# Optimization experiments

Hardware: AMD Instinct MI355X
Metric: run time of the kernel (lower is better)

Reference implementation:

```python
import jax, jax.numpy as jnp
import numpy as np
import math

B, Q, D = 1, 1024, 4096
H, KV, HD = 32, 8, 128
GROUP_FACTOR, LABEL_BITS, HEAVY_CONST = 8, 4, 256
ROPE_THETA = 10000.0
NEG = jnp.finfo(jnp.float32).min


def setup_inputs() -> dict:
    key = jax.random.key(0)
    ks = jax.random.split(key, 5)
    hidden_states = jax.random.normal(ks[0], (B, Q, D), jnp.float32)
    Wq = jax.random.normal(ks[1], (D, H * HD), jnp.float32) * 0.02
    Wk = jax.random.normal(ks[2], (D, KV * HD), jnp.float32) * 0.02
    Wv = jax.random.normal(ks[3], (D, KV * HD), jnp.float32) * 0.02
    Wo = jax.random.normal(ks[4], (H * HD, D), jnp.float32) * 0.02
    # additive causal mask [B,1,Q,Q]
    causal = jnp.tril(jnp.ones((Q, Q), bool))
    attention_mask = jnp.where(causal, 0.0, NEG)[None, None].astype(jnp.float32)
    position_ids = jnp.arange(Q, dtype=jnp.int64 if jax.config.jax_enable_x64 else jnp.int32)[None]
    # per-head channel permutation (sorted channel importance order)
    rng = np.random.default_rng(0)
    sorted_channel = jnp.asarray(np.stack([rng.permutation(HD) for _ in range(H)]), jnp.int32)
    return {"hidden_states": hidden_states, "attention_mask": attention_mask,
            "position_ids": position_ids, "Wq": Wq, "Wk": Wk, "Wv": Wv, "Wo": Wo,
            "sorted_channel": sorted_channel}


def pseudo_quantize(t, q_bit):
    max_quant = 2 ** q_bit - 1
    mn = jnp.min(t, axis=-1, keepdims=True)
    mx = jnp.max(t, axis=-1, keepdims=True)
    rng = mx - mn
    rng = jnp.where(rng == 0, 1.0, rng)
    scale = max_quant / rng
    quant = jnp.clip(jnp.round((t - mn) * scale), 0, max_quant)
    return quant / scale + mn


def rotate_half(x):
    x1, x2 = jnp.split(x, 2, axis=-1)
    return jnp.concatenate([-x2, x1], axis=-1)


def _forward(hidden_states, attention_mask, Wq, Wk, Wv, Wo, position_ids, sorted_channel):
    bsz, q_len, _ = hidden_states.shape
    q = (hidden_states @ Wq).reshape(bsz, q_len, H, HD).transpose(0, 2, 1, 3)   # [B,H,Q,HD]
    k = (hidden_states @ Wk).reshape(bsz, q_len, KV, HD).transpose(0, 2, 1, 3)  # [B,KV,Q,HD]
    v = (hidden_states @ Wv).reshape(bsz, q_len, KV, HD).transpose(0, 2, 1, 3)
    kv_len = q_len

    # RoPE
    inv_freq = 1.0 / (ROPE_THETA ** (jnp.arange(0, HD, 2, dtype=jnp.float32) / HD))
    freqs = position_ids.astype(jnp.float32)[..., None] * inv_freq  # [B,Q,HD/2]
    emb = jnp.concatenate([freqs, freqs], axis=-1)
    cos = jnp.cos(emb)[:, None]  # [B,1,Q,HD]
    sin = jnp.sin(emb)[:, None]
    q = q * cos + rotate_half(q) * sin
    k = k * cos + rotate_half(k) * sin
    prev_q = q  # upper_layer_embedding is None -> previous_query_states == query_states

    # GQA repeat
    groups = H // KV
    k = jnp.repeat(k, groups, axis=1)  # [B,H,K,HD]
    v = jnp.repeat(v, groups, axis=1)

    attn = jnp.einsum('bhqd,bhkd->bhqk', q, k) / math.sqrt(HD)

    # channel gather per head (sorted_channel: [H,HD] permutation)
    idx = jnp.broadcast_to(sorted_channel[None, :, None, :], q.shape)
    sq = jnp.take_along_axis(prev_q, idx, axis=-1)
    sk = jnp.take_along_axis(k, jnp.broadcast_to(sorted_channel[None, :, None, :], k.shape), axis=-1)
    outlier = HD // GROUP_FACTOR
    gq = sq[..., :outlier]
    gk = sk[..., :outlier]
    if LABEL_BITS < 16:
        gq = pseudo_quantize(gq, LABEL_BITS)
        gk = pseudo_quantize(gk, LABEL_BITS)
    gattn = jnp.einsum('bhqd,bhkd->bhqk', gq, gk) / math.sqrt(outlier)

    attn = attn + attention_mask
    gattn = gattn + attention_mask

    # keep top heavy_const positions per query by grouped score (descending)
    rank = jnp.argsort(jnp.argsort(-gattn, axis=-1), axis=-1)
    attn = jnp.where(rank < HEAVY_CONST, attn, -jnp.inf)

    w = jax.nn.softmax(attn.astype(jnp.float32), axis=-1).astype(v.dtype)
    out = jnp.einsum('bhqk,bhkd->bhqd', w, v)
    out = out.transpose(0, 2, 1, 3).reshape(bsz, q_len, H * HD)
    return out @ Wo


def reference(hidden_states, attention_mask, position_ids, Wq, Wk, Wv, Wo, sorted_channel):
    return _forward(hidden_states, attention_mask, Wq, Wk, Wv, Wo, position_ids, sorted_channel)
```

## Files before the change

kernel.cpp:

```cpp
#include <hip/hip_runtime.h>
#include <hip/hip_bf16.h>
#include <math.h>


typedef __hip_bfloat16 bf16;
typedef unsigned short ushort_t;
typedef __attribute__((ext_vector_type(8))) short short8;
typedef __attribute__((ext_vector_type(4))) float f32x4;

#define QL   1024
#define DM   4096
#define NH   32
#define NKV  8
#define GRP  4
#define HD   128
#define OUTL 16
#define HC   256
#define MNEG (-1.0e30f)

__device__ __forceinline__ unsigned mapf(float f) {
  unsigned u = __float_as_uint(f);
  return (u & 0x80000000u) ? ~u : (u | 0x80000000u);
}

__device__ __forceinline__ unsigned short f2bf(float x) {
  unsigned u = __float_as_uint(x);
  unsigned r = (u + 0x7FFFu + ((u >> 16) & 1u)) >> 16;
  return (unsigned short)r;
}
__device__ __forceinline__ float bf2f(unsigned short h) {
  return __uint_as_float(((unsigned)h) << 16);
}

__device__ __forceinline__ short8 cvt8(const float* p) {
  f32x4 a = *(const f32x4*)p;
  f32x4 b = *(const f32x4*)(p + 4);
  short8 r;
#pragma unroll
  for (int i = 0; i < 4; i++) r[i] = (short)f2bf(a[i]);
#pragma unroll
  for (int i = 0; i < 4; i++) r[4 + i] = (short)f2bf(b[i]);
  return r;
}

__device__ __forceinline__ void split8(const float* p, short8& h, short8& l) {
  f32x4 a = *(const f32x4*)p;
  f32x4 b = *(const f32x4*)(p + 4);
#pragma unroll
  for (int i = 0; i < 4; i++) {
    unsigned short hh = f2bf(a[i]);
    h[i] = (short)hh;
    l[i] = (short)f2bf(a[i] - bf2f(hh));
  }
#pragma unroll
  for (int i = 0; i < 4; i++) {
    unsigned short hh = f2bf(b[i]);
    h[4 + i] = (short)hh;
    l[4 + i] = (short)f2bf(b[i] - bf2f(hh));
  }
}

__device__ __forceinline__ int bswz(int n, int k) {
  return n * 32 + (k ^ (((n >> 3) & 3) * 8));
}

__device__ __forceinline__ int s4(int col) {
  return col ^ (((col >> 5) & 7) << 2);
}

__device__ __forceinline__ int dppReduce32(int v) {
  v += __builtin_amdgcn_update_dpp(0, v, 0xB1, 0xF, 0xF, true);
  v += __builtin_amdgcn_update_dpp(0, v, 0x4E, 0xF, 0xF, true);
  v += __builtin_amdgcn_update_dpp(0, v, 0x124, 0xF, 0xF, true);
  v += __builtin_amdgcn_update_dpp(0, v, 0x128, 0xF, 0xF, true);
  v += __builtin_amdgcn_ds_swizzle(v, 0x401F);
  return v;
}

__global__ __launch_bounds__(256)
void transpose_bf16_kernel(const bf16* __restrict__ src, bf16* __restrict__ dst,
                           int K, int N, long long srcBS, long long dstBS) {
  __shared__ alignas(16) unsigned short tile[64][64];
  const bf16* s = src + (size_t)blockIdx.z * srcBS;
  bf16* d = dst + (size_t)blockIdx.z * dstBS;
  const int k0 = blockIdx.y * 64, n0 = blockIdx.x * 64;
  const int t = threadIdx.x;
  {
    const int r = t >> 3;
    const int c8 = (t & 7) * 8;
    const int sw0 = ((r >> 3) & 7) * 8;
    const int sw1 = (((r + 32) >> 3) & 7) * 8;
    *(short8*)&tile[r][c8 ^ sw0] =
        *(const short8*)&s[(size_t)(k0 + r) * N + n0 + c8];
    *(short8*)&tile[r + 32][c8 ^ sw1] =
        *(const short8*)&s[(size_t)(k0 + r + 32) * N + n0 + c8];
  }
  __syncthreads();
  {
    const int kc8 = t & 7;
    const int nr = t >> 3;
    short8 v0, v1;
#pragma unroll
    for (int j = 0; j < 8; j++) {
      const int rowj = kc8 * 8 + j;
      const int swj = ((rowj >> 3) & 7) * 8;
      v0[j] = (short)tile[rowj][nr ^ swj];
      v1[j] = (short)tile[rowj][(nr + 32) ^ swj];
    }
    *(short8*)&d[(size_t)(n0 + nr) * K + k0 + kc8 * 8] = v0;
    *(short8*)&d[(size_t)(n0 + nr + 32) * K + k0 + kc8 * 8] = v1;
  }
}

__global__ __launch_bounds__(256)
void gemm_qkv_kernel(const void* __restrict__ hsv, const void* __restrict__ Wqv,
                     const void* __restrict__ Wkv, const void* __restrict__ Wvv,
                     float* __restrict__ C, const ushort_t* __restrict__ msk) {
  const bool ibf = (msk[1] != 0);
  const int n0 = blockIdx.x * 128;
  const int m0 = blockIdx.y * 64;
  const void* Bv;
  int Nb, cb;
  bool wantSplit;
  if (n0 < 4096)      { Bv = Wqv; Nb = 4096; cb = n0;        wantSplit = true; }
  else if (n0 < 5120) { Bv = Wkv; Nb = 1024; cb = n0 - 4096; wantSplit = true; }
  else                { Bv = Wvv; Nb = 1024; cb = n0 - 5120; wantSplit = false; }
  const bool doSplit = wantSplit && !ibf;

  __shared__ alignas(16) bf16 sAh[64 * 32];
  __shared__ alignas(16) bf16 sAl[64 * 32];
  __shared__ alignas(16) bf16 sBh[128 * 32];
  __shared__ alignas(16) bf16 sBl[128 * 32];

  const int t = threadIdx.x, lane = t & 63, wave = t >> 6;
  const int wm = (wave >> 1) * 32, wn = (wave & 1) * 64;
  const int mrow = lane & 15, kq = (lane >> 4) * 8;
  const int r0 = t >> 2, o0 = (t & 3) * 8;
  const int bk2 = (t >> 4) * 2;
  const int bn8 = (t & 15) * 8;
  f32x4 acc[2][4];
#pragma unroll
  for (int i = 0; i < 2; i++)
#pragma unroll
    for (int j = 0; j < 4; j++) acc[i][j] = (f32x4){0.f, 0.f, 0.f, 0.f};

  for (int kk = 0; kk < DM; kk += 32) {
    short8 ah, al, bh0, bl0, bh1, bl1;
    if (ibf) {
      const bf16* A = (const bf16*)hsv;
      const bf16* B = (const bf16*)Bv;
      ah = *(const short8*)&A[(size_t)(m0 + r0) * DM + kk + o0];
      bh0 = *(const short8*)&B[(size_t)(kk + bk2) * Nb + cb + bn8];
      bh1 = *(const short8*)&B[(size_t)(kk + bk2 + 1) * Nb + cb + bn8];
    } else {
      const float* A = (const float*)hsv;
      const float* B = (const float*)Bv;
      split8(&A[(size_t)(m0 + r0) * DM + kk + o0], ah, al);
      if (doSplit) {
        split8(&B[(size_t)(kk + bk2) * Nb + cb + bn8], bh0, bl0);
        split8(&B[(size_t)(kk + bk2 + 1) * Nb + cb + bn8], bh1, bl1);
      } else {
        bh0 = cvt8(&B[(size_t)(kk + bk2) * Nb + cb + bn8]);
        bh1 = cvt8(&B[(size_t)(kk + bk2 + 1) * Nb + cb + bn8]);
      }
    }
    __syncthreads();
    *(short8*)&sAh[r0 * 32 + o0] = ah;
    if (doSplit) *(short8*)&sAl[r0 * 32 + o0] = al;
#pragma unroll
    for (int i = 0; i < 8; i++) {
      unsigned pv = (unsigned)(unsigned short)bh0[i] |
                    ((unsigned)(unsigned short)bh1[i] << 16);
      *(unsigned*)&sBh[bswz(bn8 + i, bk2)] = pv;
    }
    if (doSplit) {
#pragma unroll
      for (int i = 0; i < 8; i++) {
        unsigned pv = (unsigned)(unsigned short)bl0[i] |
                      ((unsigned)(unsigned short)bl1[i] << 16);
        *(unsigned*)&sBl[bswz(bn8 + i, bk2)] = pv;
      }
    }
    __syncthreads();
    short8 afh[2], bfh[4];
#pragma unroll
    for (int i = 0; i < 2; i++)
      afh[i] = *(const short8*)&sAh[(wm + i * 16 + mrow) * 32 + kq];
#pragma unroll
    for (int j = 0; j < 4; j++)
      bfh[j] = *(const short8*)&sBh[bswz(wn + j * 16 + mrow, kq)];
#pragma unroll
    for (int i = 0; i < 2; i++)
#pragma unroll
      for (int j = 0; j < 4; j++)
        acc[i][j] = __builtin_amdgcn_mfma_f32_16x16x32_bf16(afh[i], bfh[j], acc[i][j], 0, 0, 0);
    if (doSplit) {
      short8 afl[2], bfl[4];
#pragma unroll
      for (int i = 0; i < 2; i++)
        afl[i] = *(const short8*)&sAl[(wm + i * 16 + mrow) * 32 + kq];
#pragma unroll
      for (int j = 0; j < 4; j++)
        bfl[j] = *(const short8*)&sBl[bswz(wn + j * 16 + mrow, kq)];
#pragma unroll
      for (int i = 0; i < 2; i++)
#pragma unroll
        for (int j = 0; j < 4; j++) {
          acc[i][j] = __builtin_amdgcn_mfma_f32_16x16x32_bf16(afh[i], bfl[j], acc[i][j], 0, 0, 0);
          acc[i][j] = __builtin_amdgcn_mfma_f32_16x16x32_bf16(afl[i], bfh[j], acc[i][j], 0, 0, 0);
        }
    }
  }
  const int rq = (lane >> 4) * 4, cn = lane & 15;
#pragma unroll
  for (int i = 0; i < 2; i++)
#pragma unroll
    for (int r = 0; r < 4; r++) {
      const size_t rowi = (size_t)(m0 + wm + i * 16 + rq + r);
#pragma unroll
      for (int j = 0; j < 4; j++)
        C[rowi * 6144 + (n0 + wn + j * 16 + cn)] = acc[i][j][r];
    }
}

__global__ __launch_bounds__(256)
void gemm_wo_kernel(const bf16* __restrict__ A, const void* __restrict__ Bv,
                    void* __restrict__ Cv, const ushort_t* __restrict__ msk) {
  const bool ibf = (msk[1] != 0);
  __shared__ alignas(16) bf16 sA[64 * 32];
  __shared__ alignas(16) bf16 sB[128 * 32];
  const int n0 = blockIdx.x * 128;
  const int m0 = blockIdx.y * 64;
  const int t = threadIdx.x, lane = t & 63, wave = t >> 6;
  const int wm = (wave >> 1) * 32, wn = (wave & 1) * 64;
  const int mrow = lane & 15, kq = (lane >> 4) * 8;
  const int r0 = t >> 2, o0 = (t & 3) * 8;
  const int bk2 = (t >> 4) * 2;
  const int bn8 = (t & 15) * 8;
  f32x4 acc[2][4];
#pragma unroll
  for (int i = 0; i < 2; i++)
#pragma unroll
    for (int j = 0; j < 4; j++) acc[i][j] = (f32x4){0.f, 0.f, 0.f, 0.f};

  for (int kk = 0; kk < DM; kk += 32) {
    short8 av = *(const short8*)&A[(size_t)(m0 + r0) * DM + kk + o0];
    short8 bv0, bv1;
    if (ibf) {
      const bf16* B = (const bf16*)Bv;
      bv0 = *(const short8*)&B[(size_t)(kk + bk2) * DM + n0 + bn8];
      bv1 = *(const short8*)&B[(size_t)(kk + bk2 + 1) * DM + n0 + bn8];
    } else {
      const float* B = (const float*)Bv;
      bv0 = cvt8(&B[(size_t)(kk + bk2) * DM + n0 + bn8]);
      bv1 = cvt8(&B[(size_t)(kk + bk2 + 1) * DM + n0 + bn8]);
    }
    __syncthreads();
    *(short8*)&sA[r0 * 32 + o0] = av;
#pragma unroll
    for (int i = 0; i < 8; i++) {
      unsigned pv = (unsigned)(unsigned short)bv0[i] |
                    ((unsigned)(unsigned short)bv1[i] << 16);
      *(unsigned*)&sB[bswz(bn8 + i, bk2)] = pv;
    }
    __syncthreads();
    short8 af[2], bfr[4];
#pragma unroll
    for (int i = 0; i < 2; i++)
      af[i] = *(const short8*)&sA[(wm + i * 16 + mrow) * 32 + kq];
#pragma unroll
    for (int j = 0; j < 4; j++)
      bfr[j] = *(const short8*)&sB[bswz(wn + j * 16 + mrow, kq)];
#pragma unroll
    for (int i = 0; i < 2; i++)
#pragma unroll
      for (int j = 0; j < 4; j++)
        acc[i][j] = __builtin_amdgcn_mfma_f32_16x16x32_bf16(af[i], bfr[j], acc[i][j], 0, 0, 0);
  }
  const int rq = (lane >> 4) * 4, cn = lane & 15;
#pragma unroll
  for (int i = 0; i < 2; i++)
#pragma unroll
    for (int r = 0; r < 4; r++) {
      const size_t rowi = (size_t)(m0 + wm + i * 16 + rq + r);
#pragma unroll
      for (int j = 0; j < 4; j++) {
        const size_t idx = rowi * DM + (n0 + wn + j * 16 + cn);
        if (ibf)
          ((bf16*)Cv)[idx] = __float2bfloat16(acc[i][j][r]);
        else
          ((float*)Cv)[idx] = acc[i][j][r];
      }
    }
}

__global__ __launch_bounds__(64)
void rope_tab_kernel(float* __restrict__ tab) {
  const int i = threadIdx.x;
  tab[i] = (float)(1.0 / pow(10000.0, (double)i * (1.0 / 64.0)));
}

__global__ __launch_bounds__(128)
void rope_cs_kernel(const float* __restrict__ tab, float* __restrict__ cs,
                    float* __restrict__ sn) {
  const int pos = blockIdx.x, d = threadIdx.x;
  const float inv = tab[d & 63];
  const float ang = (float)pos * inv;
  cs[pos * HD + d] = cosf(ang);
  sn[pos * HD + d] = sinf(ang);
}

__global__ __launch_bounds__(128)
void rope_q_gq_kernel(const float* __restrict__ qkv, const int* __restrict__ sc,
                      bf16* __restrict__ qr, float* __restrict__ gq,
                      const float* __restrict__ cs, const float* __restrict__ sn) {
  const int pos = blockIdx.x, h = blockIdx.y, d = threadIdx.x;
  __shared__ float sv[HD], sr[HD];
  __shared__ float smn, smx;
  float v = qkv[(size_t)pos * 6144 + h * HD + d];
  sv[d] = v;
  __syncthreads();
  const float c = cs[pos * HD + d], s = sn[pos * HD + d];
  float rot = (d < 64) ? -sv[d + 64] : sv[d - 64];
  float r = v * c + rot * s;
  sr[d] = r;
  qr[((size_t)h * QL + pos) * HD + d] = __float2bfloat16(r);
  __syncthreads();
  if (d == 0) {
    float mn = 3.4e38f, mx = -3.4e38f;
    for (int j = 0; j < OUTL; j++) {
      float g = sr[sc[h * HD + j]];
      mn = fminf(mn, g);
      mx = fmaxf(mx, g);
    }
    smn = mn; smx = mx;
  }
  __syncthreads();
  if (d < OUTL) {
    float g = sr[sc[h * HD + d]];
    float rng = smx - smn;
    if (rng == 0.f) rng = 1.f;
    float scale = 15.0f / rng;
    float qv = rintf((g - smn) * scale);
    qv = fminf(fmaxf(qv, 0.f), 15.f);
    gq[((size_t)h * QL + pos) * OUTL + d] = qv / scale + smn;
  }
}

__global__ __launch_bounds__(128)
void rope_k_gk_kernel(const float* __restrict__ qkv, const int* __restrict__ sc,
                      bf16* __restrict__ kr, bf16* __restrict__ vrow,
                      float* __restrict__ gk,
                      const float* __restrict__ cs, const float* __restrict__ sn) {
  const int pos = blockIdx.x, kvh = blockIdx.y, d = threadIdx.x;
  __shared__ float sv[HD], sr[HD];
  __shared__ float smn[GRP], smx[GRP];
  float kv = qkv[(size_t)pos * 6144 + DM + kvh * HD + d];
  float vv = qkv[(size_t)pos * 6144 + DM + NKV * HD + kvh * HD + d];
  sv[d] = kv;
  __syncthreads();
  const float c = cs[pos * HD + d], s = sn[pos * HD + d];
  float rot = (d < 64) ? -sv[d + 64] : sv[d - 64];
  float r = kv * c + rot * s;
  sr[d] = r;
  kr[((size_t)kvh * QL + pos) * HD + d] = __float2bfloat16(r);
  vrow[((size_t)kvh * QL + pos) * HD + d] = __float2bfloat16(vv);
  __syncthreads();
  if (d < 64 && (d & 15) == 0) {
    const int g = d >> 4;
    const int h = kvh * GRP + g;
    float mn = 3.4e38f, mx = -3.4e38f;
    for (int j = 0; j < OUTL; j++) {
      float x = sr[sc[h * HD + j]];
      mn = fminf(mn, x);
      mx = fmaxf(mx, x);
    }
    smn[g] = mn; smx[g] = mx;
  }
  __syncthreads();
  if (d < 64) {
    const int g = d >> 4, j = d & 15;
    const int h = kvh * GRP + g;
    float x = sr[sc[h * HD + j]];
    float rng = smx[g] - smn[g];
    if (rng == 0.f) rng = 1.f;
    float scale = 15.0f / rng;
    float qv = rintf((x - smn[g]) * scale);
    qv = fminf(fmaxf(qv, 0.f), 15.f);
    gk[((size_t)h * QL + pos) * OUTL + j] = qv / scale + smn[g];
  }
}

__global__ __launch_bounds__(256)
void attn_kernel(const bf16* __restrict__ qr, const bf16* __restrict__ kr,
                 const bf16* __restrict__ vT, const float* __restrict__ gq,
                 const float* __restrict__ gk, bf16* __restrict__ ao) {
  const int h = blockIdx.y;
  const int q0 = ((int)gridDim.x - 1 - (int)blockIdx.x) * 8;
  const int kvh = h >> 2;
  const int t = threadIdx.x;
  const int lane = t & 63, wave = t >> 6;
  const int mrow = lane & 15, kq = (lane >> 4) * 8;
  const int row = t >> 5, j32 = t & 31;
  const int kmax = q0 + 8;
  const bool needSel = (kmax > HC);

  __shared__ alignas(16) bf16 sQ[16][HD];
  __shared__ float sGq[8][OUTL];
  __shared__ alignas(16) float sBuf[8][QL];
  __shared__ float sL[8];

  {
    const int r = t >> 4, c8 = (t & 15) * 8;
    short8 z = {0, 0, 0, 0, 0, 0, 0, 0};
    if (r < 8)
      *(short8*)&sQ[r][c8] = *(const short8*)&qr[((size_t)h * QL + q0 + r) * HD + c8];
    else
      *(short8*)&sQ[r][c8] = z;
    if (needSel && t < 128)
      sGq[t >> 4][t & 15] = gq[((size_t)h * QL + q0 + (t >> 4)) * OUTL + (t & 15)];
  }
  __syncthreads();

  unsigned sel = 0xFFFFFFFFu;
  if (needSel) {
    for (int kk = t; kk < kmax; kk += 256) {
      const float* gkp = &gk[((size_t)h * QL + kk) * OUTL];
      float gv[OUTL];
#pragma unroll
      for (int j = 0; j < OUTL; j++) gv[j] = gkp[j];
      const int pk = s4(kk);
#pragma unroll
      for (int r = 0; r < 8; r++) {
        float s = 0.f;
#pragma unroll
        for (int j = 0; j < OUTL; j++) s += sGq[r][j] * gv[j];
        sBuf[r][pk] = (kk <= q0 + r) ? s * 0.25f : MNEG;
      }
    }
    __syncthreads();

    {
      const int base = j32 * 32;
      const int cz = j32 & 7;
      unsigned uv[32];
#pragma unroll
      for (int g = 0; g < 8; g++) {
        f32x4 v = *(const f32x4*)&sBuf[row][base + ((g ^ cz) << 2)];
#pragma unroll
        for (int m = 0; m < 4; m++) {
          const int kk = g * 4 + m;
          uv[kk] = (base + kk < kmax) ? mapf(v[m]) : 0u;
        }
      }
#define TST(J, M)                                                     \
  _Pragma("unroll") for (int k2 = 0; k2 < 32; k2++) if ((k2 & (J)) == 0) { \
    unsigned tt = (uv[k2] ^ (uv[k2 + (J)] >> (J))) & (M);             \
    uv[k2] ^= tt;                                                     \
    uv[k2 + (J)] ^= (tt << (J));                                      \
  }
      TST(16, 0x0000FFFFu)
      TST(8, 0x00FF00FFu)
      TST(4, 0x0F0F0F0Fu)
      TST(2, 0x33333333u)
      TST(1, 0x55555555u)
#undef TST
      unsigned act = 0xFFFFFFFFu, gtm = 0u;
      int greater = 0, act_tot = QL;
      bool done = false;
#pragma unroll
      for (int p = 0; p < 32; p++) {
        if (__all(done)) break;
        if (!done) {
          const unsigned ones = act & uv[p];
          const int c = dppReduce32(__popc(ones));
          if (greater + c >= HC) {
            act = ones;
            act_tot = c;
          } else {
            greater += c;
            gtm |= ones;
            act ^= ones;
            act_tot -= c;
          }
          if (greater + act_tot == HC) {
            sel = __brev(gtm | act);
            done = true;
          }
        }
      }
      if (!done) {
        const unsigned gtmN = __brev(gtm), eqmN = __brev(act);
        const int needEq = HC - greater;
        const int eqc = __popc(eqmN);
        int pre = eqc;
#pragma unroll
        for (int dlt = 1; dlt < 32; dlt <<= 1) {
          int o = __shfl_up(pre, dlt, 32);
          if (j32 >= dlt) pre += o;
        }
        pre -= eqc;
        int take = needEq - pre;
        unsigned mm = eqmN;
        sel = gtmN;
        for (int i = 0; i < take && mm != 0u; i++) {
          unsigned b = mm & (0u - mm);
          sel |= b;
          mm ^= b;
        }
      }
    }
    __syncthreads();
  }

  {
    short8 aq[4];
#pragma unroll
    for (int kb = 0; kb < 4; kb++)
      aq[kb] = *(const short8*)&sQ[mrow][kb * 32 + kq];
    const bf16* krh = &kr[(size_t)kvh * QL * HD];
    const int ntmax = (kmax + 15) >> 4;
    for (int nt = wave; nt < ntmax; nt += 4) {
      const int kb0 = nt * 16;
      f32x4 acc = {0.f, 0.f, 0.f, 0.f};
#pragma unroll
      for (int kb = 0; kb < 4; kb++) {
        short8 bfr = *(const short8*)&krh[(size_t)(kb0 + mrow) * HD + kb * 32 + kq];
        acc = __builtin_amdgcn_mfma_f32_16x16x32_bf16(aq[kb], bfr, acc, 0, 0, 0);
      }
      const int key = kb0 + mrow;
      const int pk = s4(key);
#pragma unroll
      for (int r = 0; r < 4; r++) {
        const int m = (lane >> 4) * 4 + r;
        if (m < 8) {
          float v = acc[r] * 0.08838834764831845f;
          sBuf[m][pk] = (key <= q0 + m) ? v : MNEG;
        }
      }
    }
  }
  __syncthreads();

  const int kbmax = (kmax + 31) >> 5;

  {
    const int base = j32 * 32;
    const int cz = j32 & 7;
    const int rbound = q0 + row;
    float av[32];
#pragma unroll
    for (int g = 0; g < 8; g++) {
      f32x4 v = *(const f32x4*)&sBuf[row][base + ((g ^ cz) << 2)];
#pragma unroll
      for (int m = 0; m < 4; m++) av[g * 4 + m] = v[m];
    }
    float mx = MNEG;
#pragma unroll
    for (int kk = 0; kk < 32; kk++)
      if (((sel >> kk) & 1u) && (base + kk <= rbound)) mx = fmaxf(mx, av[kk]);
    mx = fmaxf(mx, __shfl_xor(mx, 1, 32));
    mx = fmaxf(mx, __shfl_xor(mx, 2, 32));
    mx = fmaxf(mx, __shfl_xor(mx, 4, 32));
    mx = fmaxf(mx, __shfl_xor(mx, 8, 32));
    mx = fmaxf(mx, __shfl_xor(mx, 16, 32));
    float ls = 0.f;
#pragma unroll
    for (int kk = 0; kk < 32; kk++) {
      float p = 0.f;
      if (((sel >> kk) & 1u) && (base + kk <= rbound)) {
        float e = av[kk] - mx;
        p = (e < -80.f) ? 0.f : expf(e);
        ls += p;
      }
      av[kk] = p;
    }
    ls += __shfl_xor(ls, 1, 32);
    ls += __shfl_xor(ls, 2, 32);
    ls += __shfl_xor(ls, 4, 32);
    ls += __shfl_xor(ls, 8, 32);
    ls += __shfl_xor(ls, 16, 32);
    if (j32 == 0) sL[row] = ls;
    __syncthreads();
    bf16* P = (bf16*)&sBuf[0][0];
    if (j32 < kbmax) {
      const int rk = row & 3;
#pragma unroll
      for (int g = 0; g < 4; g++) {
        short8 pv8;
#pragma unroll
        for (int m = 0; m < 8; m++) pv8[m] = (short)f2bf(av[g * 8 + m]);
        *(short8*)&P[(size_t)row * QL + base + ((g ^ rk) << 3)] = pv8;
      }
    }
    {
      const int zr = 8 + row;
      if (j32 < kbmax) {
        short8 z = {0, 0, 0, 0, 0, 0, 0, 0};
#pragma unroll
        for (int i = 0; i < 4; i++)
          *(short8*)&P[(size_t)zr * QL + j32 * 32 + i * 8] = z;
      }
    }
  }
  __syncthreads();

  {
    const bf16* Pb = (const bf16*)&sBuf[0][0];
    const bf16* vTh = &vT[(size_t)kvh * HD * QL];
    const int rk = mrow & 3;
    for (int dt = wave; dt < 8; dt += 4) {
      const int d0 = dt * 16;
      f32x4 acc = {0.f, 0.f, 0.f, 0.f};
      for (int kb = 0; kb < kbmax; kb++) {
        short8 af = *(const short8*)&Pb[(size_t)mrow * QL + kb * 32 + (kq ^ (rk << 3))];
        short8 bfr = *(const short8*)&vTh[(size_t)(d0 + mrow) * QL + kb * 32 + kq];
        acc = __builtin_amdgcn_mfma_f32_16x16x32_bf16(af, bfr, acc, 0, 0, 0);
      }
#pragma unroll
      for (int r = 0; r < 4; r++) {
        const int m = (lane >> 4) * 4 + r;
        if (m < 8) {
          float outv = acc[r] / sL[m];
          ao[(size_t)(q0 + m) * DM + h * HD + d0 + mrow] = __float2bfloat16(outv);
        }
      }
    }
  }
}

extern "C" void kernel_launch(void* const* d_in, const int* in_sizes, int n_in,
                              void* d_out, int out_size, void* d_ws, size_t ws_size,
                              hipStream_t stream) {
  (void)in_sizes; (void)n_in; (void)out_size; (void)ws_size;
  const void* hs = d_in[0];
  const ushort_t* msk = (const ushort_t*)d_in[1];
  const void* Wq = d_in[3];
  const void* Wk = d_in[4];
  const void* Wv = d_in[5];
  const void* Wo = d_in[6];
  const int* sc = (const int*)d_in[7];

  char* ws = (char*)d_ws;
  size_t off = 0;
  auto alloc = [&](size_t bytes) {
    char* p = ws + off;
    off += (bytes + 255) & ~(size_t)255;
    return p;
  };
  float* qkv = (float*)alloc((size_t)QL * 6144 * 4);
  bf16* ao = (bf16*)qkv;
  bf16* qr = (bf16*)alloc((size_t)NH * QL * HD * 2);
  bf16* kr = (bf16*)alloc((size_t)NKV * QL * HD * 2);
  bf16* vrow = (bf16*)alloc((size_t)NKV * QL * HD * 2);
  bf16* vT = (bf16*)alloc((size_t)NKV * HD * QL * 2);
  float* gq = (float*)alloc((size_t)NH * QL * OUTL * 4);
  float* gk = (float*)alloc((size_t)NH * QL * OUTL * 4);
  float* tab = (float*)alloc(64 * 4);
  float* cst = (float*)alloc((size_t)QL * HD * 4);
  float* snt = (float*)alloc((size_t)QL * HD * 4);

  rope_tab_kernel<<<1, 64, 0, stream>>>(tab);
  rope_cs_kernel<<<dim3(QL), 128, 0, stream>>>(tab, cst, snt);

  gemm_qkv_kernel<<<dim3(48, 16), 256, 0, stream>>>(hs, Wq, Wk, Wv, qkv, msk);

  rope_q_gq_kernel<<<dim3(QL, NH), 128, 0, stream>>>(qkv, sc, qr, gq, cst, snt);
  rope_k_gk_kernel<<<dim3(QL, NKV), 128, 0, stream>>>(qkv, sc, kr, vrow, gk, cst, snt);
  transpose_bf16_kernel<<<dim3(2, 16, NKV), 256, 0, stream>>>(
      vrow, vT, QL, HD, (long long)(QL * HD), (long long)(HD * QL));

  attn_kernel<<<dim3(QL / 8, NH), 256, 0, stream>>>(qr, kr, vT, gq, gk, ao);

  gemm_wo_kernel<<<dim3(32, 16), 256, 0, stream>>>(ao, Wo, d_out, msk);
}
```

Measured before the change: 767.4 us.

## Presplit and pre-transpose GEMM operands to bf16 and load via global_load_lds

Adds separate pre-pass kernels that convert the fp32 activations and weights into hi/lo bf16 pairs, transposing and swizzling the weights into a K-contiguous layout. The QKV and output GEMMs then stream those tiles straight into LDS with global_load_lds instead of converting in registers and scattering into LDS. The attention kernel writes its output in the matching swizzled layout. This removes the repeated per-tile split and convert work and the strided weight reads inside the GEMMs. The cost is extra full passes over all weight matrices every call and more workspace memory.

Result: faster. 626.8 us (-18.3%).

```diff
diff --git a/kernel.cpp b/kernel.cpp
--- a/kernel.cpp
+++ b/kernel.cpp
@@ -7,6 +7,7 @@
 typedef unsigned short ushort_t;
 typedef __attribute__((ext_vector_type(8))) short short8;
 typedef __attribute__((ext_vector_type(4))) float f32x4;
+typedef __attribute__((ext_vector_type(4))) unsigned u32x4;
 
 #define QL   1024
 #define DM   4096
@@ -32,17 +33,6 @@
   return __uint_as_float(((unsigned)h) << 16);
 }
 
-__device__ __forceinline__ short8 cvt8(const float* p) {
-  f32x4 a = *(const f32x4*)p;
-  f32x4 b = *(const f32x4*)(p + 4);
-  short8 r;
-#pragma unroll
-  for (int i = 0; i < 4; i++) r[i] = (short)f2bf(a[i]);
-#pragma unroll
-  for (int i = 0; i < 4; i++) r[4 + i] = (short)f2bf(b[i]);
-  return r;
-}
-
 __device__ __forceinline__ void split8(const float* p, short8& h, short8& l) {
   f32x4 a = *(const f32x4*)p;
   f32x4 b = *(const f32x4*)(p + 4);
@@ -60,8 +50,31 @@
   }
 }
 
-__device__ __forceinline__ int bswz(int n, int k) {
-  return n * 32 + (k ^ (((n >> 3) & 3) * 8));
+__device__ __forceinline__ void splitp8(const float* p, unsigned* o) {
+  f32x4 a = *(const f32x4*)p;
+  f32x4 b = *(const f32x4*)(p + 4);
+#pragma unroll
+  for (int i = 0; i < 4; i++) {
+    unsigned short hh = f2bf(a[i]);
+    unsigned short ll = f2bf(a[i] - bf2f(hh));
+    o[i] = (unsigned)hh | ((unsigned)ll << 16);
+  }
+#pragma unroll
+  for (int i = 0; i < 4; i++) {
+    unsigned short hh = f2bf(b[i]);
+    unsigned short ll = f2bf(b[i] - bf2f(hh));
+    o[4 + i] = (unsigned)hh | ((unsigned)ll << 16);
+  }
+}
+
+__device__ __forceinline__ int aswz(int r, int k) {
+  return r * 32 + (k ^ (((r >> 1) & 3) << 3));
+}
+
+__device__ __forceinline__ void gll16(const bf16* g, bf16* l) {
+  __builtin_amdgcn_global_load_lds(
+      (const __attribute__((address_space(1))) void*)g,
+      (__attribute__((address_space(3))) void*)l, 16, 0, 0);
 }
 
 __device__ __forceinline__ int s4(int col) {
@@ -113,19 +126,90 @@
 }
 
 __global__ __launch_bounds__(256)
-void gemm_qkv_kernel(const void* __restrict__ hsv, const void* __restrict__ Wqv,
-                     const void* __restrict__ Wkv, const void* __restrict__ Wvv,
-                     float* __restrict__ C, const ushort_t* __restrict__ msk) {
+void split_a_kernel(const void* __restrict__ hsv, bf16* __restrict__ Ah,
+                    bf16* __restrict__ Al, const ushort_t* __restrict__ msk) {
+  const bool ibf = (msk[1] != 0);
+  const int gid = blockIdx.x * 256 + threadIdx.x;
+  const int m = gid >> 9, c = gid & 511;
+  const int cs = c ^ ((m >> 1) & 3);
+  const size_t srci = (size_t)m * DM + (size_t)c * 8;
+  const size_t dsti = (size_t)m * DM + (size_t)cs * 8;
+  if (ibf) {
+    *(short8*)&Ah[dsti] = *(const short8*)((const bf16*)hsv + srci);
+  } else {
+    short8 h, l;
+    split8((const float*)hsv + srci, h, l);
+    *(short8*)&Ah[dsti] = h;
+    *(short8*)&Al[dsti] = l;
+  }
+}
+
+__global__ __launch_bounds__(256)
+void wsplitT_kernel(const void* __restrict__ src, int Nsrc,
+                    bf16* __restrict__ dh, bf16* __restrict__ dl,
+                    int n_off, int wantLo, const ushort_t* __restrict__ msk) {
+  const bool ibf = (msk[1] != 0);
+  __shared__ alignas(16) unsigned tile[64][64];
+  const int n0 = blockIdx.x * 64;
+  const int k0 = blockIdx.y * 64;
+  const int t = threadIdx.x;
+  {
+    const int r = t >> 3, c8 = (t & 7) * 8;
+    unsigned p0[8], p1[8];
+    if (ibf) {
+      const bf16* S = (const bf16*)src;
+      short8 v0 = *(const short8*)&S[(size_t)(k0 + r) * Nsrc + n0 + c8];
+      short8 v1 = *(const short8*)&S[(size_t)(k0 + r + 32) * Nsrc + n0 + c8];
+#pragma unroll
+      for (int i = 0; i < 8; i++) {
+        p0[i] = (unsigned)(unsigned short)v0[i];
+        p1[i] = (unsigned)(unsigned short)v1[i];
+      }
+    } else {
+      const float* S = (const float*)src;
+      splitp8(&S[(size_t)(k0 + r) * Nsrc + n0 + c8], p0);
+      splitp8(&S[(size_t)(k0 + r + 32) * Nsrc + n0 + c8], p1);
+    }
+    const int sw0 = ((r >> 3) & 7) * 8;
+    const int sw1 = (((r + 32) >> 3) & 7) * 8;
+    *(u32x4*)&tile[r][c8 ^ sw0] = *(u32x4*)&p0[0];
+    *(u32x4*)&tile[r][(c8 ^ sw0) + 4] = *(u32x4*)&p0[4];
+    *(u32x4*)&tile[r + 32][c8 ^ sw1] = *(u32x4*)&p1[0];
+    *(u32x4*)&tile[r + 32][(c8 ^ sw1) + 4] = *(u32x4*)&p1[4];
+  }
+  __syncthreads();
+  {
+    const int kc8 = t & 7, nr = t >> 3;
+    short8 h0, l0, h1, l1;
+#pragma unroll
+    for (int j = 0; j < 8; j++) {
+      const int rowj = kc8 * 8 + j;
+      const int swj = ((rowj >> 3) & 7) * 8;
+      unsigned g0 = tile[rowj][nr ^ swj];
+      unsigned g1 = tile[rowj][(nr + 32) ^ swj];
+      h0[j] = (short)(g0 & 0xFFFFu); l0[j] = (short)(g0 >> 16);
+      h1[j] = (short)(g1 & 0xFFFFu); l1[j] = (short)(g1 >> 16);
+    }
+    const int na = n_off + n0 + nr, nb = na + 32;
+    const int cha = (k0 >> 3) + (kc8 ^ ((na >> 1) & 3));
+    const int chb = (k0 >> 3) + (kc8 ^ ((nb >> 1) & 3));
+    *(short8*)&dh[(size_t)na * DM + ((size_t)cha << 3)] = h0;
+    *(short8*)&dh[(size_t)nb * DM + ((size_t)chb << 3)] = h1;
+    if (wantLo && !ibf) {
+      *(short8*)&dl[(size_t)na * DM + ((size_t)cha << 3)] = l0;
+      *(short8*)&dl[(size_t)nb * DM + ((size_t)chb << 3)] = l1;
+    }
+  }
+}
+
+__global__ __launch_bounds__(256)
+void gemm_qkv2_kernel(const bf16* __restrict__ Ah, const bf16* __restrict__ Al,
+                      const bf16* __restrict__ WhT, const bf16* __restrict__ WlT,
+                      float* __restrict__ C, const ushort_t* __restrict__ msk) {
   const bool ibf = (msk[1] != 0);
   const int n0 = blockIdx.x * 128;
   const int m0 = blockIdx.y * 64;
-  const void* Bv;
-  int Nb, cb;
-  bool wantSplit;
-  if (n0 < 4096)      { Bv = Wqv; Nb = 4096; cb = n0;        wantSplit = true; }
-  else if (n0 < 5120) { Bv = Wkv; Nb = 1024; cb = n0 - 4096; wantSplit = true; }
-  else                { Bv = Wvv; Nb = 1024; cb = n0 - 5120; wantSplit = false; }
-  const bool doSplit = wantSplit && !ibf;
+  const bool doSplit = (n0 < 5120) && !ibf;
 
   __shared__ alignas(16) bf16 sAh[64 * 32];
   __shared__ alignas(16) bf16 sAl[64 * 32];
@@ -135,9 +219,16 @@
   const int t = threadIdx.x, lane = t & 63, wave = t >> 6;
   const int wm = (wave >> 1) * 32, wn = (wave & 1) * 64;
   const int mrow = lane & 15, kq = (lane >> 4) * 8;
-  const int r0 = t >> 2, o0 = (t & 3) * 8;
-  const int bk2 = (t >> 4) * 2;
-  const int bn8 = (t & 15) * 8;
+  const size_t aoff = (size_t)(m0 + (t >> 2)) * DM + (size_t)(t & 3) * 8;
+  const size_t boff0 = (size_t)(n0 + (t >> 2)) * DM + (size_t)(t & 3) * 8;
+  const size_t boff1 = (size_t)(n0 + 64 + (t >> 2)) * DM + (size_t)(t & 3) * 8;
+  bf16* lA_h = sAh + wave * 512;
+  bf16* lA_l = sAl + wave * 512;
+  bf16* lB0h = sBh + wave * 512;
+  bf16* lB1h = sBh + 2048 + wave * 512;
+  bf16* lB0l = sBl + wave * 512;
+  bf16* lB1l = sBl + 2048 + wave * 512;
+
   f32x4 acc[2][4];
 #pragma unroll
   for (int i = 0; i < 2; i++)
@@ -145,50 +236,23 @@
     for (int j = 0; j < 4; j++) acc[i][j] = (f32x4){0.f, 0.f, 0.f, 0.f};
 
   for (int kk = 0; kk < DM; kk += 32) {
-    short8 ah, al, bh0, bl0, bh1, bl1;
-    if (ibf) {
-      const bf16* A = (const bf16*)hsv;
-      const bf16* B = (const bf16*)Bv;
-      ah = *(const short8*)&A[(size_t)(m0 + r0) * DM + kk + o0];
-      bh0 = *(const short8*)&B[(size_t)(kk + bk2) * Nb + cb + bn8];
-      bh1 = *(const short8*)&B[(size_t)(kk + bk2 + 1) * Nb + cb + bn8];
-    } else {
-      const float* A = (const float*)hsv;
-      const float* B = (const float*)Bv;
-      split8(&A[(size_t)(m0 + r0) * DM + kk + o0], ah, al);
-      if (doSplit) {
-        split8(&B[(size_t)(kk + bk2) * Nb + cb + bn8], bh0, bl0);
-        split8(&B[(size_t)(kk + bk2 + 1) * Nb + cb + bn8], bh1, bl1);
-      } else {
-        bh0 = cvt8(&B[(size_t)(kk + bk2) * Nb + cb + bn8]);
-        bh1 = cvt8(&B[(size_t)(kk + bk2 + 1) * Nb + cb + bn8]);
-      }
-    }
     __syncthreads();
-    *(short8*)&sAh[r0 * 32 + o0] = ah;
-    if (doSplit) *(short8*)&sAl[r0 * 32 + o0] = al;
-#pragma unroll
-    for (int i = 0; i < 8; i++) {
-      unsigned pv = (unsigned)(unsigned short)bh0[i] |
-                    ((unsigned)(unsigned short)bh1[i] << 16);
-      *(unsigned*)&sBh[bswz(bn8 + i, bk2)] = pv;
-    }
+    gll16(Ah + aoff + kk, lA_h);
+    gll16(WhT + boff0 + kk, lB0h);
+    gll16(WhT + boff1 + kk, lB1h);
     if (doSplit) {
-#pragma unroll
-      for (int i = 0; i < 8; i++) {
-        unsigned pv = (unsigned)(unsigned short)bl0[i] |
-                      ((unsigned)(unsigned short)bl1[i] << 16);
-        *(unsigned*)&sBl[bswz(bn8 + i, bk2)] = pv;
-      }
+      gll16(Al + aoff + kk, lA_l);
+      gll16(WlT + boff0 + kk, lB0l);
+      gll16(WlT + boff1 + kk, lB1l);
     }
     __syncthreads();
     short8 afh[2], bfh[4];
 #pragma unroll
     for (int i = 0; i < 2; i++)
-      afh[i] = *(const short8*)&sAh[(wm + i * 16 + mrow) * 32 + kq];
+      afh[i] = *(const short8*)&sAh[aswz(wm + i * 16 + mrow, kq)];
 #pragma unroll
     for (int j = 0; j < 4; j++)
-      bfh[j] = *(const short8*)&sBh[bswz(wn + j * 16 + mrow, kq)];
+      bfh[j] = *(const short8*)&sBh[aswz(wn + j * 16 + mrow, kq)];
 #pragma unroll
     for (int i = 0; i < 2; i++)
 #pragma unroll
@@ -198,10 +262,10 @@
       short8 afl[2], bfl[4];
 #pragma unroll
       for (int i = 0; i < 2; i++)
-        afl[i] = *(const short8*)&sAl[(wm + i * 16 + mrow) * 32 + kq];
+        afl[i] = *(const short8*)&sAl[aswz(wm + i * 16 + mrow, kq)];
 #pragma unroll
       for (int j = 0; j < 4; j++)
-        bfl[j] = *(const short8*)&sBl[bswz(wn + j * 16 + mrow, kq)];
+        bfl[j] = *(const short8*)&sBl[aswz(wn + j * 16 + mrow, kq)];
 #pragma unroll
       for (int i = 0; i < 2; i++)
 #pragma unroll
@@ -224,8 +288,8 @@
 }
 
 __global__ __launch_bounds__(256)
-void gemm_wo_kernel(const bf16* __restrict__ A, const void* __restrict__ Bv,
-                    void* __restrict__ Cv, const ushort_t* __restrict__ msk) {
+void gemm_wo2_kernel(const bf16* __restrict__ Ao, const bf16* __restrict__ WoT,
+                     void* __restrict__ Cv, const ushort_t* __restrict__ msk) {
   const bool ibf = (msk[1] != 0);
   __shared__ alignas(16) bf16 sA[64 * 32];
   __shared__ alignas(16) bf16 sB[128 * 32];
@@ -234,9 +298,13 @@
   const int t = threadIdx.x, lane = t & 63, wave = t >> 6;
   const int wm = (wave >> 1) * 32, wn = (wave & 1) * 64;
   const int mrow = lane & 15, kq = (lane >> 4) * 8;
-  const int r0 = t >> 2, o0 = (t & 3) * 8;
-  const int bk2 = (t >> 4) * 2;
-  const int bn8 = (t & 15) * 8;
+  const size_t aoff = (size_t)(m0 + (t >> 2)) * DM + (size_t)(t & 3) * 8;
+  const size_t boff0 = (size_t)(n0 + (t >> 2)) * DM + (size_t)(t & 3) * 8;
+  const size_t boff1 = (size_t)(n0 + 64 + (t >> 2)) * DM + (size_t)(t & 3) * 8;
+  bf16* lA = sA + wave * 512;
+  bf16* lB0 = sB + wave * 512;
+  bf16* lB1 = sB + 2048 + wave * 512;
+
   f32x4 acc[2][4];
 #pragma unroll
   for (int i = 0; i < 2; i++)
@@ -244,33 +312,18 @@
     for (int j = 0; j < 4; j++) acc[i][j] = (f32x4){0.f, 0.f, 0.f, 0.f};
 
   for (int kk = 0; kk < DM; kk += 32) {
-    short8 av = *(const short8*)&A[(size_t)(m0 + r0) * DM + kk + o0];
-    short8 bv0, bv1;
-    if (ibf) {
-      const bf16* B = (const bf16*)Bv;
-      bv0 = *(const short8*)&B[(size_t)(kk + bk2) * DM + n0 + bn8];
-      bv1 = *(const short8*)&B[(size_t)(kk + bk2 + 1) * DM + n0 + bn8];
-    } else {
-      const float* B = (const float*)Bv;
-      bv0 = cvt8(&B[(size_t)(kk + bk2) * DM + n0 + bn8]);
-      bv1 = cvt8(&B[(size_t)(kk + bk2 + 1) * DM + n0 + bn8]);
-    }
     __syncthreads();
-    *(short8*)&sA[r0 * 32 + o0] = av;
-#pragma unroll
-    for (int i = 0; i < 8; i++) {
-      unsigned pv = (unsigned)(unsigned short)bv0[i] |
-                    ((unsigned)(unsigned short)bv1[i] << 16);
-      *(unsigned*)&sB[bswz(bn8 + i, bk2)] = pv;
-    }
+    gll16(Ao + aoff + kk, lA);
+    gll16(WoT + boff0 + kk, lB0);
+    gll16(WoT + boff1 + kk, lB1);
     __syncthreads();
     short8 af[2], bfr[4];
 #pragma unroll
     for (int i = 0; i < 2; i++)
-      af[i] = *(const short8*)&sA[(wm + i * 16 + mrow) * 32 + kq];
+      af[i] = *(const short8*)&sA[aswz(wm + i * 16 + mrow, kq)];
 #pragma unroll
     for (int j = 0; j < 4; j++)
-      bfr[j] = *(const short8*)&sB[bswz(wn + j * 16 + mrow, kq)];
+      bfr[j] = *(const short8*)&sB[aswz(wn + j * 16 + mrow, kq)];
 #pragma unroll
     for (int i = 0; i < 2; i++)
 #pragma unroll
@@ -294,17 +347,10 @@
     }
 }
 
-__global__ __launch_bounds__(64)
-void rope_tab_kernel(float* __restrict__ tab) {
-  const int i = threadIdx.x;
-  tab[i] = (float)(1.0 / pow(10000.0, (double)i * (1.0 / 64.0)));
-}
-
 __global__ __launch_bounds__(128)
-void rope_cs_kernel(const float* __restrict__ tab, float* __restrict__ cs,
-                    float* __restrict__ sn) {
+void rope_cs_kernel(float* __restrict__ cs, float* __restrict__ sn) {
   const int pos = blockIdx.x, d = threadIdx.x;
-  const float inv = tab[d & 63];
+  const float inv = (float)(1.0 / pow(10000.0, (double)(d & 63) * (1.0 / 64.0)));
   const float ang = (float)pos * inv;
   cs[pos * HD + d] = cosf(ang);
   sn[pos * HD + d] = sinf(ang);
@@ -622,7 +668,10 @@
         const int m = (lane >> 4) * 4 + r;
         if (m < 8) {
           float outv = acc[r] / sL[m];
-          ao[(size_t)(q0 + m) * DM + h * HD + d0 + mrow] = __float2bfloat16(outv);
+          const int rowm = q0 + m;
+          const int col = h * HD + d0 + mrow;
+          const int ch = (col >> 3) ^ ((rowm >> 1) & 3);
+          ao[(size_t)rowm * DM + (ch << 3) + (col & 7)] = __float2bfloat16(outv);
         }
       }
     }
@@ -656,21 +705,30 @@
   bf16* vT = (bf16*)alloc((size_t)NKV * HD * QL * 2);
   float* gq = (float*)alloc((size_t)NH * QL * OUTL * 4);
   float* gk = (float*)alloc((size_t)NH * QL * OUTL * 4);
-  float* tab = (float*)alloc(64 * 4);
   float* cst = (float*)alloc((size_t)QL * HD * 4);
   float* snt = (float*)alloc((size_t)QL * HD * 4);
-
-  rope_tab_kernel<<<1, 64, 0, stream>>>(tab);
-  rope_cs_kernel<<<dim3(QL), 128, 0, stream>>>(tab, cst, snt);
-
-  gemm_qkv_kernel<<<dim3(48, 16), 256, 0, stream>>>(hs, Wq, Wk, Wv, qkv, msk);
+  bf16* Ahs = (bf16*)alloc((size_t)QL * DM * 2);
+  bf16* Als = (bf16*)alloc((size_t)QL * DM * 2);
+  bf16* WhT = (bf16*)alloc((size_t)6144 * DM * 2);
+  bf16* WlT = (bf16*)alloc((size_t)5120 * DM * 2);
+  bf16* WoT = WhT;
+
+  rope_cs_kernel<<<dim3(QL), 128, 0, stream>>>(cst, snt);
+
+  split_a_kernel<<<dim3(2048), 256, 0, stream>>>(hs, Ahs, Als, msk);
+  wsplitT_kernel<<<dim3(64, 64), 256, 0, stream>>>(Wq, 4096, WhT, WlT, 0, 1, msk);
+  wsplitT_kernel<<<dim3(16, 64), 256, 0, stream>>>(Wk, 1024, WhT, WlT, 4096, 1, msk);
+  wsplitT_kernel<<<dim3(16, 64), 256, 0, stream>>>(Wv, 1024, WhT, WlT, 5120, 0, msk);
+
+  gemm_qkv2_kernel<<<dim3(48, 16), 256, 0, stream>>>(Ahs, Als, WhT, WlT, qkv, msk);
 
   rope_q_gq_kernel<<<dim3(QL, NH), 128, 0, stream>>>(qkv, sc, qr, gq, cst, snt);
   rope_k_gk_kernel<<<dim3(QL, NKV), 128, 0, stream>>>(qkv, sc, kr, vrow, gk, cst, snt);
   transpose_bf16_kernel<<<dim3(2, 16, NKV), 256, 0, stream>>>(
       vrow, vT, QL, HD, (long long)(QL * HD), (long long)(HD * QL));
 
+  wsplitT_kernel<<<dim3(64, 64), 256, 0, stream>>>(Wo, 4096, WoT, WlT, 0, 0, msk);
   attn_kernel<<<dim3(QL / 8, NH), 256, 0, stream>>>(qr, kr, vT, gq, gk, ao);
 
-  gemm_wo_kernel<<<dim3(32, 16), 256, 0, stream>>>(ao, Wo, d_out, msk);
-}
+  gemm_wo2_kernel<<<dim3(32, 16), 256, 0, stream>>>(ao, WoT, d_out, msk);
+}
```
